# Kernel optimization log

Hardware: AMD Instinct MI355X
Metric: run time of the kernel (lower is better)

Reference implementation:

```python
import jax, jax.numpy as jnp
import numpy as np

N = 8388608      # number of points
S = 32768        # number of superpoints (segments)


def setup_inputs() -> dict:
    key = jax.random.key(0)
    k1, k2, k3 = jax.random.split(key, 3)
    pos = jax.random.normal(k1, (N, 3), dtype=jnp.float32)
    idx = jnp.sort(jax.random.randint(k2, (N,), 0, S, dtype=jnp.int64))
    w = jax.random.uniform(k3, (N,), dtype=jnp.float32)  # non-negative weights
    return {"pos": pos, "idx": idx, "w": w, "num_super": S}


def reference(pos, idx, w, num_super):
    # Per-segment min / max of coordinates: [S, 3]
    mn = jax.ops.segment_min(pos, idx, num_segments=num_super, indices_are_sorted=True)
    mx = jax.ops.segment_max(pos, idx, num_segments=num_super, indices_are_sorted=True)
    # Per-segment diameter = largest coordinate extent: [S]
    diameter_segment = (mx - mn).max(axis=1)
    # Weighted per-segment center: sum(w*pos) / sum(w), guarding zero-weight segments
    w_sum = jax.ops.segment_sum(w, idx, num_segments=num_super, indices_are_sorted=True)
    w_sum_safe = jnp.where(w_sum == 0, 1.0, w_sum)
    center_segment = (
        jax.ops.segment_sum(pos * w[:, None], idx, num_segments=num_super,
                            indices_are_sorted=True)
        / w_sum_safe[:, None]
    )
    # Gather per-node center/diameter and normalize into unit sphere
    pos_out = (pos - center_segment[idx]) / (diameter_segment[idx][:, None] + 0.01)
    return pos_out, diameter_segment.reshape(-1, 1)
```

## Files before the change

### kernel.cpp

```cpp
#include <hip/hip_runtime.h>

#define WAVE 64
#define WPB 2

template <int CTRL>
__device__ __forceinline__ float dpp_f(float x) {
    int xi = __builtin_bit_cast(int, x);
    int r  = __builtin_amdgcn_update_dpp(xi, xi, CTRL, 0xF, 0xF, false);
    return __builtin_bit_cast(float, r);
}
#define DPP_XOR1 0xB1
#define DPP_XOR2 0x4E
#define DPP_XOR4 0x141
#define DPP_XOR8 0x140

__global__ void detect_idx64(const unsigned int* __restrict__ w32, long long N,
                             int* __restrict__ flag) {
    long long base = (N / 2) | 1LL;
    long long stride = ((N / 2) / 64) & ~1LL;
    if (stride < 2) stride = 2;
    long long p = base + (long long)threadIdx.x * stride;
    unsigned int v = (p < N) ? w32[p] : 0u;
    unsigned long long nz = __ballot(v != 0u);
    if (threadIdx.x == 0) *flag = (nz == 0ULL) ? 1 : 0;
}

__device__ __forceinline__ int load_idx(const void* __restrict__ p,
                                        long long i, int is64) {
    return is64 ? (int)((const long long*)p)[i] : ((const int*)p)[i];
}

__global__ void find_bounds_bs(const void* __restrict__ idxp,
                               const int* __restrict__ flag,
                               int* __restrict__ start,
                               long long N, int S) {
    const int t = blockIdx.x * blockDim.x + threadIdx.x;
    if (t > S) return;
    const int is64 = *flag;
    long long lo = 0, hi = N;
    while (lo < hi) {
        long long mid = (lo + hi) >> 1;
        if (load_idx(idxp, mid, is64) < t) lo = mid + 1; else hi = mid;
    }
    start[t] = (int)lo;
}

__global__ __launch_bounds__(WPB * WAVE)
void seg_norm(const float* __restrict__ pos,
              const float* __restrict__ w,
              const int* __restrict__ start,
              float* __restrict__ out,
              float* __restrict__ diam_out,
              int S) {
    const int s = blockIdx.x * WPB + (threadIdx.x >> 6);
    if (s >= S) return;
    const int lane = threadIdx.x & 63;

    const int lo = start[s], hi = start[s + 1];
    const int g0 = lo >> 2, g1 = (hi + 3) >> 2;

    const float4* __restrict__ pos4 = (const float4*)pos;
    const float4* __restrict__ w4   = (const float4*)w;

    const int ga = g0 + lane;
    const int gb = ga + WAVE;
    const bool va = ga < g1, vb = gb < g1;
    const bool anyb = __any(vb);

    float4 a0 = {0,0,0,0}, a1 = {0,0,0,0}, a2 = {0,0,0,0}, aw = {0,0,0,0};
    float4 b0 = {0,0,0,0}, b1 = {0,0,0,0}, b2 = {0,0,0,0}, bw = {0,0,0,0};
    if (va) {
        a0 = pos4[3LL * ga]; a1 = pos4[3LL * ga + 1]; a2 = pos4[3LL * ga + 2];
        aw = w4[ga];
    }
    if (vb) {
        b0 = pos4[3LL * gb]; b1 = pos4[3LL * gb + 1]; b2 = pos4[3LL * gb + 2];
        bw = w4[gb];
    }

    float mnx = INFINITY,  mny = INFINITY,  mnz = INFINITY;
    float mxx = -INFINITY, mxy = -INFINITY, mxz = -INFINITY;
    float sw = 0.f, swx = 0.f, swy = 0.f, swz = 0.f;

    #define PROC(PI, X, Y, Z, WV)                                        \
    {                                                                    \
        bool in = ((PI) >= lo) & ((PI) < hi);                            \
        float xv = (X), yv = (Y), zv = (Z);                              \
        float wv = in ? (WV) : 0.f;                                      \
        mnx = fminf(mnx, in ? xv :  INFINITY);                           \
        mxx = fmaxf(mxx, in ? xv : -INFINITY);                           \
        mny = fminf(mny, in ? yv :  INFINITY);                           \
        mxy = fmaxf(mxy, in ? yv : -INFINITY);                           \
        mnz = fminf(mnz, in ? zv :  INFINITY);                           \
        mxz = fmaxf(mxz, in ? zv : -INFINITY);                           \
        sw += wv;                                                        \
        swx = fmaf(wv, xv, swx);                                         \
        swy = fmaf(wv, yv, swy);                                         \
        swz = fmaf(wv, zv, swz);                                         \
    }
    #define PROC_GROUP(G, R0, R1, R2, RW)                                \
    {                                                                    \
        const int p = (G) << 2;                                          \
        PROC(p + 0, R0.x, R0.y, R0.z, RW.x)                              \
        PROC(p + 1, R0.w, R1.x, R1.y, RW.y)                              \
        PROC(p + 2, R1.z, R1.w, R2.x, RW.z)                              \
        PROC(p + 3, R2.y, R2.z, R2.w, RW.w)                              \
    }

    PROC_GROUP(ga, a0, a1, a2, aw)
    if (anyb) PROC_GROUP(gb, b0, b1, b2, bw)

    for (int g = g0 + 2 * WAVE + lane; g < g1; g += WAVE) {
        float4 c0 = pos4[3LL * g], c1 = pos4[3LL * g + 1], c2 = pos4[3LL * g + 2];
        float4 cw = w4[g];
        PROC_GROUP(g, c0, c1, c2, cw)
    }

    #define ALLV(STAGEOP)                                \
        mnx = fminf(mnx, STAGEOP(mnx));                  \
        mny = fminf(mny, STAGEOP(mny));                  \
        mnz = fminf(mnz, STAGEOP(mnz));                  \
        mxx = fmaxf(mxx, STAGEOP(mxx));                  \
        mxy = fmaxf(mxy, STAGEOP(mxy));                  \
        mxz = fmaxf(mxz, STAGEOP(mxz));                  \
        sw  += STAGEOP(sw);                              \
        swx += STAGEOP(swx);                             \
        swy += STAGEOP(swy);                             \
        swz += STAGEOP(swz);
    #define ST_X1(v)  dpp_f<DPP_XOR1>(v)
    #define ST_X2(v)  dpp_f<DPP_XOR2>(v)
    #define ST_X4(v)  dpp_f<DPP_XOR4>(v)
    #define ST_X8(v)  dpp_f<DPP_XOR8>(v)
    #define ST_X16(v) __shfl_xor((v), 16)
    #define ST_X32(v) __shfl_xor((v), 32)
    ALLV(ST_X1)
    ALLV(ST_X2)
    ALLV(ST_X4)
    ALLV(ST_X8)
    ALLV(ST_X16)
    ALLV(ST_X32)
    #undef ST_X1
    #undef ST_X2
    #undef ST_X4
    #undef ST_X8
    #undef ST_X16
    #undef ST_X32
    #undef ALLV

    const float diam = fmaxf(mxx - mnx, fmaxf(mxy - mny, mxz - mnz));
    const float wsafe = (sw == 0.f) ? 1.f : sw;
    const float cx = swx / wsafe, cy = swy / wsafe, cz = swz / wsafe;
    const float inv = 1.f / (diam + 0.01f);
    if (lane == 0) diam_out[s] = diam;

    float4* __restrict__ out4 = (float4*)out;

    #define STORE_GROUP(G, R0, R1, R2)                                       \
    {                                                                        \
        const int p = (G) << 2;                                              \
        float4 ra, rb, rc;                                                   \
        ra.x = (R0.x - cx) * inv; ra.y = (R0.y - cy) * inv;                  \
        ra.z = (R0.z - cz) * inv; ra.w = (R0.w - cx) * inv;                  \
        rb.x = (R1.x - cy) * inv; rb.y = (R1.y - cz) * inv;                  \
        rb.z = (R1.z - cx) * inv; rb.w = (R1.w - cy) * inv;                  \
        rc.x = (R2.x - cz) * inv; rc.y = (R2.y - cx) * inv;                  \
        rc.z = (R2.z - cy) * inv; rc.w = (R2.w - cz) * inv;                  \
        if (p >= lo && p + 4 <= hi) {                                        \
            out4[3LL * (G)] = ra; out4[3LL * (G) + 1] = rb;                  \
            out4[3LL * (G) + 2] = rc;                                        \
        } else {                                                             \
            const long long f = 12LL * (G);                                  \
            if (p + 0 >= lo && p + 0 < hi) {                                 \
                out[f + 0] = ra.x; out[f + 1]  = ra.y; out[f + 2]  = ra.z;   \
            }                                                                \
            if (p + 1 >= lo && p + 1 < hi) {                                 \
                out[f + 3] = ra.w; out[f + 4]  = rb.x; out[f + 5]  = rb.y;   \
            }                                                                \
            if (p + 2 >= lo && p + 2 < hi) {                                 \
                out[f + 6] = rb.z; out[f + 7]  = rb.w; out[f + 8]  = rc.x;   \
            }                                                                \
            if (p + 3 >= lo && p + 3 < hi) {                                 \
                out[f + 9] = rc.y; out[f + 10] = rc.z; out[f + 11] = rc.w;   \
            }                                                                \
        }                                                                    \
    }

    STORE_GROUP(ga, a0, a1, a2)
    if (anyb) STORE_GROUP(gb, b0, b1, b2)

    for (int g = g0 + 2 * WAVE + lane; g < g1; g += WAVE) {
        float4 c0 = pos4[3LL * g], c1 = pos4[3LL * g + 1], c2 = pos4[3LL * g + 2];
        STORE_GROUP(g, c0, c1, c2)
    }

    #undef STORE_GROUP
    #undef PROC_GROUP
    #undef PROC
}

extern "C" void kernel_launch(void* const* d_in, const int* in_sizes, int n_in,
                              void* d_out, int out_size, void* d_ws, size_t ws_size,
                              hipStream_t stream) {
    const float* pos  = (const float*)d_in[0];
    const void*  idxp = d_in[1];
    const float* w    = (const float*)d_in[2];

    const long long N = (long long)in_sizes[0] / 3;
    const int S = out_size - in_sizes[0];

    float* out = (float*)d_out;
    float* diam_out = out + (long long)in_sizes[0];

    int* flag  = (int*)d_ws;
    int* start = (int*)((char*)d_ws + 256);

    detect_idx64<<<1, 64, 0, stream>>>((const unsigned int*)idxp, N, flag);

    find_bounds_bs<<<(S + 1 + 63) / 64, 64, 0, stream>>>(idxp, flag, start, N, S);

    seg_norm<<<(S + WPB - 1) / WPB, WPB * WAVE, 0, stream>>>(
        pos, w, start, out, diam_out, S);
}
```

Before: 57.10 us.

## Split segment stats and normalization into separate dense-pass kernels

The fused per-segment kernel, which reread pos and wrote the normalized output per segment, is split in two. The first kernel now only computes per-segment center, inverse diameter and diameter into a workspace. A new flat, fully coalesced kernel then rereads pos as float4 and finds each point's segment through shared-memory lookups of segment bounds. The aim is to remove the unaligned, branchy per-segment stores and uneven per-wave work, at the cost of an extra kernel launch and extra global reads of the stats and start arrays.

```diff
diff --git a/kernel.cpp b/kernel.cpp
--- a/kernel.cpp
+++ b/kernel.cpp
@@ -2,6 +2,7 @@
 
 #define WAVE 64
 #define WPB 2
+#define CAP 48
 
 template <int CTRL>
 __device__ __forceinline__ float dpp_f(float x) {
@@ -13,6 +14,10 @@
 #define DPP_XOR2 0x4E
 #define DPP_XOR4 0x141
 #define DPP_XOR8 0x140
+
+__device__ __forceinline__ unsigned div3u(unsigned n) {
+    return (unsigned)(((unsigned long long)n * 0xAAAAAAABull) >> 33);
+}
 
 __global__ void detect_idx64(const unsigned int* __restrict__ w32, long long N,
                              int* __restrict__ flag) {
@@ -46,12 +51,12 @@
 }
 
 __global__ __launch_bounds__(WPB * WAVE)
-void seg_norm(const float* __restrict__ pos,
-              const float* __restrict__ w,
-              const int* __restrict__ start,
-              float* __restrict__ out,
-              float* __restrict__ diam_out,
-              int S) {
+void seg_stats(const float* __restrict__ pos,
+               const float* __restrict__ w,
+               const int* __restrict__ start,
+               float4* __restrict__ sseg,
+               float* __restrict__ diam_out,
+               int S) {
     const int s = blockIdx.x * WPB + (threadIdx.x >> 6);
     if (s >= S) return;
     const int lane = threadIdx.x & 63;
@@ -115,6 +120,8 @@
         float4 cw = w4[g];
         PROC_GROUP(g, c0, c1, c2, cw)
     }
+    #undef PROC_GROUP
+    #undef PROC
 
     #define ALLV(STAGEOP)                                \
         mnx = fminf(mnx, STAGEOP(mnx));                  \
@@ -133,12 +140,7 @@
     #define ST_X8(v)  dpp_f<DPP_XOR8>(v)
     #define ST_X16(v) __shfl_xor((v), 16)
     #define ST_X32(v) __shfl_xor((v), 32)
-    ALLV(ST_X1)
-    ALLV(ST_X2)
-    ALLV(ST_X4)
-    ALLV(ST_X8)
-    ALLV(ST_X16)
-    ALLV(ST_X32)
+    ALLV(ST_X1) ALLV(ST_X2) ALLV(ST_X4) ALLV(ST_X8) ALLV(ST_X16) ALLV(ST_X32)
     #undef ST_X1
     #undef ST_X2
     #undef ST_X4
@@ -147,55 +149,123 @@
     #undef ST_X32
     #undef ALLV
 
-    const float diam = fmaxf(mxx - mnx, fmaxf(mxy - mny, mxz - mnz));
-    const float wsafe = (sw == 0.f) ? 1.f : sw;
-    const float cx = swx / wsafe, cy = swy / wsafe, cz = swz / wsafe;
-    const float inv = 1.f / (diam + 0.01f);
-    if (lane == 0) diam_out[s] = diam;
-
-    float4* __restrict__ out4 = (float4*)out;
-
-    #define STORE_GROUP(G, R0, R1, R2)                                       \
-    {                                                                        \
-        const int p = (G) << 2;                                              \
-        float4 ra, rb, rc;                                                   \
-        ra.x = (R0.x - cx) * inv; ra.y = (R0.y - cy) * inv;                  \
-        ra.z = (R0.z - cz) * inv; ra.w = (R0.w - cx) * inv;                  \
-        rb.x = (R1.x - cy) * inv; rb.y = (R1.y - cz) * inv;                  \
-        rb.z = (R1.z - cx) * inv; rb.w = (R1.w - cy) * inv;                  \
-        rc.x = (R2.x - cz) * inv; rc.y = (R2.y - cx) * inv;                  \
-        rc.z = (R2.z - cy) * inv; rc.w = (R2.w - cz) * inv;                  \
-        if (p >= lo && p + 4 <= hi) {                                        \
-            out4[3LL * (G)] = ra; out4[3LL * (G) + 1] = rb;                  \
-            out4[3LL * (G) + 2] = rc;                                        \
-        } else {                                                             \
-            const long long f = 12LL * (G);                                  \
-            if (p + 0 >= lo && p + 0 < hi) {                                 \
-                out[f + 0] = ra.x; out[f + 1]  = ra.y; out[f + 2]  = ra.z;   \
-            }                                                                \
-            if (p + 1 >= lo && p + 1 < hi) {                                 \
-                out[f + 3] = ra.w; out[f + 4]  = rb.x; out[f + 5]  = rb.y;   \
-            }                                                                \
-            if (p + 2 >= lo && p + 2 < hi) {                                 \
-                out[f + 6] = rb.z; out[f + 7]  = rb.w; out[f + 8]  = rc.x;   \
-            }                                                                \
-            if (p + 3 >= lo && p + 3 < hi) {                                 \
-                out[f + 9] = rc.y; out[f + 10] = rc.z; out[f + 11] = rc.w;   \
-            }                                                                \
-        }                                                                    \
-    }
-
-    STORE_GROUP(ga, a0, a1, a2)
-    if (anyb) STORE_GROUP(gb, b0, b1, b2)
-
-    for (int g = g0 + 2 * WAVE + lane; g < g1; g += WAVE) {
-        float4 c0 = pos4[3LL * g], c1 = pos4[3LL * g + 1], c2 = pos4[3LL * g + 2];
-        STORE_GROUP(g, c0, c1, c2)
-    }
-
-    #undef STORE_GROUP
-    #undef PROC_GROUP
-    #undef PROC
+    if (lane == 0) {
+        const float diam = fmaxf(mxx - mnx, fmaxf(mxy - mny, mxz - mnz));
+        const float wsafe = (sw == 0.f) ? 1.f : sw;
+        sseg[s] = make_float4(swx / wsafe, swy / wsafe, swz / wsafe,
+                              1.f / (diam + 0.01f));
+        diam_out[s] = diam;
+    }
+}
+
+__global__ __launch_bounds__(256)
+void normalize_dense(const float* __restrict__ pos,
+                     const int* __restrict__ start,
+                     const float4* __restrict__ sseg,
+                     float* __restrict__ out,
+                     long long nF, int S) {
+    const long long nQ = nF >> 2;
+    const long long f  = (long long)blockIdx.x * 256 + threadIdx.x;
+
+    __shared__ int    sLo_sh, nb_sh, ovf_sh;
+    __shared__ int    sb[CAP];
+    __shared__ float4 sg[CAP + 1];
+
+    const long long fblk0 = (long long)blockIdx.x * 256 * 4;
+    long long fblk1 = fblk0 + 256 * 4;
+    if (fblk1 > nF) fblk1 = nF;
+    if (fblk0 >= nF) return;
+    const unsigned ptA = div3u((unsigned)fblk0);
+    const unsigned ptB = div3u((unsigned)(fblk1 - 1));
+
+    if (threadIdx.x == 0) {
+        int lo = 0, hi = S + 1;
+        while (lo + 1 < hi) {
+            int mid = (lo + hi) >> 1;
+            if ((unsigned)start[mid] <= ptA) lo = mid; else hi = mid;
+        }
+        sLo_sh = lo;
+    }
+    __syncthreads();
+    const int sLo = sLo_sh;
+
+    if (threadIdx.x < CAP) {
+        int j = sLo + 1 + threadIdx.x;
+        int b = (j <= S) ? start[j] : 0x7FFFFFFF;
+        sb[threadIdx.x] = b;
+        bool in = (j <= S) && ((unsigned)b <= ptB);
+        unsigned long long m = __ballot(in);
+        if (threadIdx.x == 0) {
+            int cnt = __popcll(m);
+            nb_sh  = cnt;
+            ovf_sh = (cnt >= CAP) ? 1 : 0;
+        }
+    }
+    __syncthreads();
+    const int nb = nb_sh;
+    if (threadIdx.x <= nb && threadIdx.x <= CAP) {
+        int j = sLo + threadIdx.x;
+        sg[threadIdx.x] = (j < S) ? sseg[j] : make_float4(0.f, 0.f, 0.f, 0.f);
+    }
+    __syncthreads();
+
+    if (f >= nQ) {
+        const long long r0 = nQ << 2;
+        const long long Fi = r0 + (f - nQ);
+        if (f == nQ && Fi < nF) {
+            for (long long q = Fi; q < nF; ++q) {
+                unsigned pt = div3u((unsigned)q);
+                int k = (int)((unsigned)q - 3u * pt);
+                int sl = 0;
+                for (int j = 0; j < nb; ++j) sl += (pt >= (unsigned)sb[j]);
+                float4 g = sg[sl];
+                float ctr = (k == 0) ? g.x : ((k == 1) ? g.y : g.z);
+                out[q] = (pos[q] - ctr) * g.w;
+            }
+        }
+        return;
+    }
+
+    const float4 q = ((const float4*)pos)[f];
+    const unsigned Fi0 = (unsigned)(f << 2);
+    const unsigned ptL = div3u(Fi0);
+    const unsigned ptH = ptL + 1;
+
+    int slL, slH;
+    if (!ovf_sh) {
+        slL = 0;
+        #pragma unroll 8
+        for (int j = 0; j < nb; ++j) slL += (ptL >= (unsigned)sb[j]);
+        slH = slL + ((slL < nb) && (ptH >= (unsigned)sb[slL]) ? 1 : 0);
+    } else {
+        int lo = 0, hi = S + 1;
+        while (lo + 1 < hi) {
+            int mid = (lo + hi) >> 1;
+            if ((unsigned)start[mid] <= ptL) lo = mid; else hi = mid;
+        }
+        slL = lo - sLo; slH = slL;
+        if ((unsigned)start[(lo + 1 <= S) ? lo + 1 : S] <= ptH && lo + 1 <= S)
+            slH = slL + 1;
+    }
+    const float4 gL = sg[slL];
+    const float4 gH = sg[slH];
+
+    float4 r;
+    {
+        const unsigned lim = 3u * ptH;
+        #pragma unroll
+        for (int c = 0; c < 4; ++c) {
+            const unsigned Fi = Fi0 + (unsigned)c;
+            const bool hiPt = (Fi >= lim);
+            const float4 g = hiPt ? gH : gL;
+            const unsigned pt = hiPt ? ptH : ptL;
+            const int k = (int)(Fi - 3u * pt);
+            const float ctr = (k == 0) ? g.x : ((k == 1) ? g.y : g.z);
+            const float v = (c == 0) ? q.x : (c == 1) ? q.y : (c == 2) ? q.z : q.w;
+            ((float*)&r)[c] = (v - ctr) * g.w;
+        }
+    }
+    ((float4*)out)[f] = r;
 }
 
 extern "C" void kernel_launch(void* const* d_in, const int* in_sizes, int n_in,
@@ -205,19 +275,26 @@
     const void*  idxp = d_in[1];
     const float* w    = (const float*)d_in[2];
 
-    const long long N = (long long)in_sizes[0] / 3;
+    const long long nF = (long long)in_sizes[0];
+    const long long N  = nF / 3;
     const int S = out_size - in_sizes[0];
 
     float* out = (float*)d_out;
-    float* diam_out = out + (long long)in_sizes[0];
+    float* diam_out = out + nF;
 
     int* flag  = (int*)d_ws;
     int* start = (int*)((char*)d_ws + 256);
+    size_t seg_off = (256 + (size_t)(S + 1) * 4 + 255) & ~(size_t)255;
+    float4* sseg = (float4*)((char*)d_ws + seg_off);
 
     detect_idx64<<<1, 64, 0, stream>>>((const unsigned int*)idxp, N, flag);
 
     find_bounds_bs<<<(S + 1 + 63) / 64, 64, 0, stream>>>(idxp, flag, start, N, S);
 
-    seg_norm<<<(S + WPB - 1) / WPB, WPB * WAVE, 0, stream>>>(
-        pos, w, start, out, diam_out, S);
-}
+    seg_stats<<<(S + WPB - 1) / WPB, WPB * WAVE, 0, stream>>>(
+        pos, w, start, sseg, diam_out, S);
+
+    const long long nQ = (nF + 3) >> 2;
+    normalize_dense<<<(int)((nQ + 255) / 256), 256, 0, stream>>>(
+        pos, start, sseg, out, nF, S);
+}
```

Measured after the change: 88.90 us. 55.7% more time.
